# Kernel optimization log

Hardware: AMD Instinct MI355X
Metric: run time of the kernel (lower is better)

Reference implementation:

```python
import jax, jax.numpy as jnp
import numpy as np
from jax import lax

RATIOS = np.array([0.5, 1.0, 2.0], dtype=np.float32)
SCALES = np.array([8.0, 16.0, 32.0], dtype=np.float32)
BASE = 16.0
FEAT_STRIDE = 16
N_PRE_NMS = 6000
N_POST_NMS = 300
NMS_THRESH = 0.7
MIN_SIZE = 16.0
SCALE = 1.0
NEG_INF = -1e30


def generate_anchor_base():
    # (y1, x1, y2, x2) anchors centered at (BASE/2, BASE/2)
    h = BASE * SCALES[None, :] * np.sqrt(RATIOS)[:, None]          # [3,3]
    w = BASE * SCALES[None, :] * np.sqrt(1.0 / RATIOS)[:, None]
    cy = cx = BASE / 2.0
    ab = np.stack([cy - h / 2, cx - w / 2, cy + h / 2, cx + w / 2], axis=-1)
    return jnp.asarray(ab.reshape(-1, 4), dtype=jnp.float32)       # [9,4]


def enumerate_shift_anchor(anchor_base, hh, ww):
    sy = jnp.arange(hh, dtype=jnp.float32) * FEAT_STRIDE
    sx = jnp.arange(ww, dtype=jnp.float32) * FEAT_STRIDE
    mx, my = jnp.meshgrid(sx, sy)                                   # np.meshgrid(shift_x, shift_y)
    shift = jnp.stack([my.ravel(), mx.ravel(), my.ravel(), mx.ravel()], axis=1)  # [K,4]
    return (shift[:, None, :] + anchor_base[None, :, :]).reshape(-1, 4)          # [K*9,4]


def conv2d(x, w, b, pad):
    y = lax.conv_general_dilated(x, w, (1, 1), [(pad, pad), (pad, pad)],
                                 dimension_numbers=('NCHW', 'OIHW', 'NCHW'))
    return y + b[None, :, None, None]


def loc2bbox(anchor, loc):
    h = anchor[:, 2] - anchor[:, 0]
    w = anchor[:, 3] - anchor[:, 1]
    cy = anchor[:, 0] + 0.5 * h
    cx = anchor[:, 1] + 0.5 * w
    dy, dx, dh, dw = loc[:, 0], loc[:, 1], loc[:, 2], loc[:, 3]
    ncy = dy * h + cy
    ncx = dx * w + cx
    nh = jnp.exp(dh) * h
    nw = jnp.exp(dw) * w
    return jnp.stack([ncy - 0.5 * nh, ncx - 0.5 * nw, ncy + 0.5 * nh, ncx + 0.5 * nw], axis=1)


def nms_fixed(boxes, scores):
    # boxes [P,4] already score-sorted desc; greedy NMS, fixed N_POST_NMS outputs (zero-padded)
    def body(i, state):
        sc, keep = state
        idx = jnp.argmax(sc)
        valid = sc[idx] > NEG_INF / 2
        keep = keep.at[i].set(jnp.where(valid, idx, -1))
        box = boxes[idx]
        tl = jnp.maximum(box[:2], boxes[:, :2])
        br = jnp.minimum(box[2:], boxes[:, 2:])
        wh = jnp.clip(br - tl, 0.0)
        inter = wh[:, 0] * wh[:, 1]
        a1 = (box[2] - box[0]) * (box[3] - box[1])
        a2 = (boxes[:, 2] - boxes[:, 0]) * (boxes[:, 3] - boxes[:, 1])
        iou = inter / jnp.maximum(a1 + a2 - inter, 1e-6)
        sc = jnp.where(iou > NMS_THRESH, NEG_INF, sc)
        sc = sc.at[idx].set(NEG_INF)
        return sc, keep
    keep = jnp.full((N_POST_NMS,), -1, dtype=jnp.int32)
    _, keep = lax.fori_loop(0, N_POST_NMS, body, (scores, keep))
    rois = boxes[jnp.maximum(keep, 0)]
    return jnp.where(keep[:, None] >= 0, rois, 0.0)                # [N_POST,4]


def propose_one(loc, fg_score, anchor, img_h, img_w):
    roi = loc2bbox(anchor, loc)                                     # [A,4]
    roi = jnp.stack([jnp.clip(roi[:, 0], 0.0, img_h),
                     jnp.clip(roi[:, 1], 0.0, img_w),
                     jnp.clip(roi[:, 2], 0.0, img_h),
                     jnp.clip(roi[:, 3], 0.0, img_w)], axis=1)
    min_size = MIN_SIZE * SCALE
    hs = roi[:, 2] - roi[:, 0]
    ws = roi[:, 3] - roi[:, 1]
    valid = (hs >= min_size) & (ws >= min_size)
    sc = jnp.where(valid, fg_score, NEG_INF)
    top_sc, top_idx = lax.top_k(sc, N_PRE_NMS)
    return nms_fixed(roi[top_idx], top_sc)


def reference(x, conv1_w, conv1_b, score_w, score_b, loc_w, loc_b, img_h, img_w):
    n, _, hh, ww = x.shape
    anchor = enumerate_shift_anchor(generate_anchor_base(), hh, ww)  # [hh*ww*9,4]
    n_anchor = anchor.shape[0] // (hh * ww)
    feat = jax.nn.relu(conv2d(x, conv1_w, conv1_b, 1))
    rpn_locs = conv2d(feat, loc_w, loc_b, 0).transpose(0, 2, 3, 1).reshape(n, -1, 4)
    rpn_scores = conv2d(feat, score_w, score_b, 0).transpose(0, 2, 3, 1)
    soft = jax.nn.softmax(rpn_scores.reshape(n, hh, ww, n_anchor, 2), axis=4)
    rpn_fg = soft[..., 1].reshape(n, -1)
    rpn_scores = rpn_scores.reshape(n, -1, 2)
    rois = jax.vmap(lambda l, s: propose_one(l, s, anchor, float(img_h), float(img_w)))(rpn_locs, rpn_fg)
    return rpn_locs, rpn_scores, rois, anchor


def setup_inputs() -> dict:
    key = jax.random.key(0)
    ks = jax.random.split(key, 4)
    return {
        'x': jax.random.normal(ks[0], (4, 512, 64, 64), dtype=jnp.float32),
        'conv1_w': jax.random.normal(ks[1], (512, 512, 3, 3), dtype=jnp.float32) * 0.01,
        'conv1_b': jnp.zeros((512,), dtype=jnp.float32),
        'score_w': jax.random.normal(ks[2], (18, 512, 1, 1), dtype=jnp.float32) * 0.01,
        'score_b': jnp.zeros((18,), dtype=jnp.float32),
        'loc_w': jax.random.normal(ks[3], (36, 512, 1, 1), dtype=jnp.float32) * 0.01,
        'loc_b': jnp.zeros((36,), dtype=jnp.float32),
        'img_h': 1024,
        'img_w': 1024,
    }
```

## Files before the change

kernel.cpp:

```cpp
#include <hip/hip_runtime.h>
#include <stdint.h>

typedef unsigned int u32;
typedef unsigned long long u64;
typedef unsigned short ushort_t;

#define NANCH 36864
#define NPRE 6000
#define NPOST 300
#define CAP 6144
#define NKEEP 6000
#define MROWS 6016
#define MW 192
#define NEG_INF_F (-1e30f)

typedef __attribute__((ext_vector_type(8))) __bf16 bf8_t;
typedef __attribute__((ext_vector_type(8))) unsigned short us8_t;
typedef __attribute__((ext_vector_type(16))) float f32x16;

union pun8 { us8_t u; bf8_t b; };

__device__ __forceinline__ u32 fsort(float f) {
    u32 u = __float_as_uint(f);
    return (u & 0x80000000u) ? ~u : (u | 0x80000000u);
}

__device__ __forceinline__ unsigned short f2bf(float f) {
    u32 u = __float_as_uint(f);
    u32 r = (u + 0x7FFFu + ((u >> 16) & 1u)) >> 16;
    return (unsigned short)r;
}
__device__ __forceinline__ float bf2f(unsigned short s) {
    return __uint_as_float(((u32)s) << 16);
}

__device__ __forceinline__ int ctz32(u32 x) {
    return __builtin_ctz(x ? x : 1u);
}

__global__ void init_k(u32* cnt) {
    if (threadIdx.x < 8) cnt[threadIdx.x] = 0u;
}

__global__ void wpack_k(const float* __restrict__ w, ushort_t* __restrict__ Wp) {
    int T = blockIdx.x * 256 + threadIdx.x;
    if (T >= 32768) return;
    int lane31 = T & 31;
    int cot    = (T >> 5) & 15;
    int khalf  = (T >> 9) & 1;
    int kc     = T >> 10;
    int co  = cot * 32 + lane31;
    int ci0 = kc * 16 + khalf * 8;
    int lane = lane31 + khalf * 32;
    const float* wr = w + (size_t)co * 4608 + (size_t)ci0 * 9;
    us8_t* P = (us8_t*)Wp;
    const size_t sa_stride = (size_t)9 * 32 * 16 * 64;
#pragma unroll
    for (int t = 0; t < 9; ++t) {
        us8_t vh, vm, vl;
#pragma unroll
        for (int j = 0; j < 8; ++j) {
            float v = wr[j * 9 + t];
            unsigned short h = f2bf(v); float r1 = v - bf2f(h);
            unsigned short m = f2bf(r1); float r2 = r1 - bf2f(m);
            vh[j] = h; vm[j] = m; vl[j] = f2bf(r2);
        }
        size_t base = ((((size_t)t) * 32 + kc) * 16 + cot) * 64 + lane;
        P[base] = vh;
        P[base + sa_stride] = vm;
        P[base + 2 * sa_stride] = vl;
    }
}

__global__ void tw1_k(const float* __restrict__ sw, const float* __restrict__ lw,
                      float* __restrict__ wt1) {
    int i = blockIdx.x * 256 + threadIdx.x;
    if (i >= 512 * 64) return;
    int ci = i >> 6;
    int ch = i & 63;
    float v = 0.f;
    if (ch < 18) v = sw[ch * 512 + ci];
    else if (ch < 54) v = lw[(ch - 18) * 512 + ci];
    wt1[i] = v;
}

__global__ __launch_bounds__(256, 2) void conv_mfma_k(const float* __restrict__ x,
                                                      const ushort_t* __restrict__ Wp,
                                                      const float* __restrict__ bias,
                                                      float* __restrict__ feat,
                                                      int img_base) {
    __shared__ __align__(16) unsigned short xs[3 * 6336];

    const int bid = blockIdx.x;
    const int xcd = bid & 7;
    const int rest = bid >> 3;
    const int rest_max = gridDim.x >> 3;
    const int coq = xcd >> 1;
    const int g = (xcd & 1) * rest_max + rest;
    const int fimg = g >> 5;
    const int hp = g & 31;
    const int n = img_base + fimg;
    const int h0 = hp * 2;

    const int tid = threadIdx.x;
    const int lane = tid & 63;
    const int wv = tid >> 6;
    const int r = wv >> 1;
    const int wb = (wv & 1) * 32;
    const int col31 = lane & 31;
    const int halfk = lane >> 5;

    f32x16 acc[4];
#pragma unroll
    for (int q = 0; q < 4; ++q)
#pragma unroll
        for (int i = 0; i < 16; ++i) acc[q][i] = 0.f;

    const us8_t* Pw = (const us8_t*)Wp;
    const size_t sa_stride = (size_t)9 * 32 * 16 * 64;
    static const int sal[6] = {0, 0, 1, 0, 1, 2};
    static const int sbl[6] = {0, 1, 0, 2, 1, 0};

    for (int kc = 0; kc < 32; ++kc) {
        for (int e = tid; e < 528; e += 256) {
            int half = e & 1;
            int rc = e >> 1;
            int rr = rc / 66;
            int cc = rc - rr * 66;
            int gr = h0 + rr - 1;
            int gc = cc - 1;
            bool inb = ((unsigned)gr < 64u) && ((unsigned)gc < 64u);
            int ci0 = kc * 16 + half * 8;
            const float* xp = x + ((((size_t)n * 512 + ci0) * 64 + gr) * 64 + gc);
            us8_t vh, vm, vl;
#pragma unroll
            for (int j = 0; j < 8; ++j) {
                float v = inb ? xp[(size_t)j * 4096] : 0.f;
                unsigned short h = f2bf(v); float r1 = v - bf2f(h);
                unsigned short m = f2bf(r1); float r2 = r1 - bf2f(m);
                vh[j] = h; vm[j] = m; vl[j] = f2bf(r2);
            }
            int off = (rr * 66 + cc) * 24 + half * 8;
            *(us8_t*)&xs[off] = vh;
            *(us8_t*)&xs[6336 + off] = vm;
            *(us8_t*)&xs[12672 + off] = vl;
        }
        __syncthreads();

#pragma unroll
        for (int t = 0; t < 9; ++t) {
            const int kh = t / 3, kw = t - kh * 3;
            pun8 Bf[3];
            int boff = ((r + kh) * 66 + (wb + col31 + kw)) * 24 + halfk * 8;
#pragma unroll
            for (int sb = 0; sb < 3; ++sb)
                Bf[sb].u = *(const us8_t*)&xs[sb * 6336 + boff];
            pun8 Af[3][4];
            size_t abase = (((size_t)t * 32 + kc) * 16 + coq * 4) * 64 + lane;
#pragma unroll
            for (int sa = 0; sa < 3; ++sa)
#pragma unroll
                for (int q = 0; q < 4; ++q)
                    Af[sa][q].u = Pw[sa * sa_stride + abase + (size_t)q * 64];
#pragma unroll
            for (int pp = 0; pp < 6; ++pp) {
                const int sa = sal[pp], sb = sbl[pp];
#pragma unroll
                for (int q = 0; q < 4; ++q)
                    acc[q] = __builtin_amdgcn_mfma_f32_32x32x16_bf16(
                        Af[sa][q].b, Bf[sb].b, acc[q], 0, 0, 0);
            }
        }
        __syncthreads();
    }

#pragma unroll
    for (int q = 0; q < 4; ++q) {
#pragma unroll
        for (int i = 0; i < 16; ++i) {
            int m = (i & 3) + 8 * (i >> 2) + 4 * halfk;
            int co = coq * 128 + q * 32 + m;
            float v = acc[q][i] + bias[co];
            v = v > 0.f ? v : 0.f;
            feat[(((size_t)fimg * 512 + co) * 64 + (h0 + r)) * 64 + (wb + col31)] = v;
        }
    }
}

__global__ __launch_bounds__(64) void head_k(const float* __restrict__ feat,
                                             const float* __restrict__ wt1,
                                             const float* __restrict__ sb,
                                             const float* __restrict__ lb,
                                             const int* __restrict__ img_h,
                                             const int* __restrict__ img_w,
                                             float* __restrict__ out_loc,
                                             float* __restrict__ out_sc,
                                             float* __restrict__ boxes,
                                             float* __restrict__ scf,
                                             int img_base) {
    const int lane = threadIdx.x;
    const int row = blockIdx.x;
    const int fimg = blockIdx.y;
    const int n = img_base + fimg;

    float acc[56];
#pragma unroll
    for (int i = 0; i < 56; i++) acc[i] = 0.f;

    for (int ci = 0; ci < 512; ++ci) {
        float f = feat[(((size_t)fimg * 512 + ci) * 64 + row) * 64 + lane];
        const float4* wp = (const float4*)(wt1 + ci * 64);
#pragma unroll
        for (int q = 0; q < 14; q++) {
            float4 w4 = wp[q];
            acc[q * 4 + 0] = fmaf(f, w4.x, acc[q * 4 + 0]);
            acc[q * 4 + 1] = fmaf(f, w4.y, acc[q * 4 + 1]);
            acc[q * 4 + 2] = fmaf(f, w4.z, acc[q * 4 + 2]);
            acc[q * 4 + 3] = fmaf(f, w4.w, acc[q * 4 + 3]);
        }
    }

    float ihf = (float)img_h[0];
    float iwf = (float)img_w[0];
    int p = row * 64 + lane;
    size_t base = (size_t)n * NANCH + (size_t)p * 9;
    float sy = 16.f * (float)row;
    float sx = 16.f * (float)lane;
    const float rat[3] = {0.5f, 1.f, 2.f};
    const float scl[3] = {8.f, 16.f, 32.f};

#pragma unroll
    for (int a = 0; a < 9; a++) {
        int rr = a / 3, s = a % 3;
        float hh = 16.f * scl[s] * sqrtf(rat[rr]);
        float wwv = 16.f * scl[s] * sqrtf(1.f / rat[rr]);
        float ab0 = 8.f - 0.5f * hh, ab1 = 8.f - 0.5f * wwv;
        float ab2 = 8.f + 0.5f * hh, ab3 = 8.f + 0.5f * wwv;
        float a0 = sy + ab0, a1c = sx + ab1, a2 = sy + ab2, a3 = sx + ab3;

        float s0 = acc[a * 2 + 0] + sb[a * 2 + 0];
        float s1 = acc[a * 2 + 1] + sb[a * 2 + 1];
        ((float2*)out_sc)[base + a] = make_float2(s0, s1);
        float m = fmaxf(s0, s1);
        float e0 = expf(s0 - m), e1 = expf(s1 - m);
        float fg = e1 / (e0 + e1);

        float dy = acc[18 + a * 4 + 0] + lb[a * 4 + 0];
        float dx = acc[18 + a * 4 + 1] + lb[a * 4 + 1];
        float dh = acc[18 + a * 4 + 2] + lb[a * 4 + 2];
        float dw = acc[18 + a * 4 + 3] + lb[a * 4 + 3];
        ((float4*)out_loc)[base + a] = make_float4(dy, dx, dh, dw);

        float h_ = a2 - a0, w_ = a3 - a1c;
        float cy = a0 + 0.5f * h_, cx = a1c + 0.5f * w_;
        float ncy = dy * h_ + cy, ncx = dx * w_ + cx;
        float nh = expf(dh) * h_, nw = expf(dw) * w_;
        float y1 = ncy - 0.5f * nh, x1 = ncx - 0.5f * nw;
        float y2 = ncy + 0.5f * nh, x2 = ncx + 0.5f * nw;
        y1 = fminf(fmaxf(y1, 0.f), ihf);
        x1 = fminf(fmaxf(x1, 0.f), iwf);
        y2 = fminf(fmaxf(y2, 0.f), ihf);
        x2 = fminf(fmaxf(x2, 0.f), iwf);
        float hs = y2 - y1, wsz = x2 - x1;
        bool valid = (hs >= 16.f) && (wsz >= 16.f);
        ((float4*)boxes)[base + a] = make_float4(y1, x1, y2, x2);
        scf[base + a] = valid ? fg : NEG_INF_F;
    }
}

__global__ void anch_k(float* __restrict__ out_anchor) {
    int i = blockIdx.x * 256 + threadIdx.x;
    if (i >= NANCH) return;
    int p = i / 9, a = i - p * 9;
    int y = p / 64, xq = p - y * 64;
    int r = a / 3, s = a - r * 3;
    const float rat[3] = {0.5f, 1.f, 2.f};
    const float scl[3] = {8.f, 16.f, 32.f};
    float hh = 16.f * scl[s] * sqrtf(rat[r]);
    float wwv = 16.f * scl[s] * sqrtf(1.f / rat[r]);
    float ab0 = 8.f - 0.5f * hh, ab1 = 8.f - 0.5f * wwv;
    float ab2 = 8.f + 0.5f * hh, ab3 = 8.f + 0.5f * wwv;
    float sy = 16.f * (float)y, sx = 16.f * (float)xq;
    ((float4*)out_anchor)[i] = make_float4(sy + ab0, sx + ab1, sy + ab2, sx + ab3);
}

__global__ __launch_bounds__(1024) void radix_k(const float* __restrict__ scf, u32* __restrict__ uT) {
    const int b = blockIdx.x;
    const int tid = threadIdx.x;
    const float* s = scf + (size_t)b * NANCH;
    __shared__ u32 hist[256];
    __shared__ u32 sel_prefix;
    __shared__ int sel_rank;
    if (tid == 0) { sel_prefix = 0u; sel_rank = NPRE; }
    __syncthreads();
    for (int p = 3; p >= 0; --p) {
        for (int i = tid; i < 256; i += 1024) hist[i] = 0u;
        __syncthreads();
        u32 prefix = sel_prefix;
        u32 highmask = (p == 3) ? 0u : (0xFFFFFFFFu << ((p + 1) * 8));
        for (int i = tid; i < NANCH; i += 1024) {
            u32 u = fsort(s[i]);
            if ((u & highmask) == prefix)
                atomicAdd(&hist[(u >> (p * 8)) & 255], 1u);
        }
        __syncthreads();
        if (tid == 0) {
            int r = sel_rank;
            u32 accum = 0;
            int bsel = 0;
            for (int bb = 255; bb >= 0; --bb) {
                accum += hist[bb];
                if ((int)accum >= r) {
                    bsel = bb;
                    sel_rank = r - (int)(accum - hist[bb]);
                    break;
                }
            }
            sel_prefix = prefix | ((u32)bsel << (p * 8));
        }
        __syncthreads();
    }
    if (tid == 0) uT[b] = sel_prefix;
}

__global__ void compact_k(const float* __restrict__ scf, const u32* __restrict__ uT,
                          u32* __restrict__ cnt, u32* __restrict__ cidx) {
    int b = blockIdx.y;
    int i = blockIdx.x * 256 + threadIdx.x;
    float s = scf[(size_t)b * NANCH + i];
    u32 u = fsort(s);
    if (u >= uT[b] && s > -5e29f) {
        u32 p = atomicAdd(&cnt[b], 1u);
        if (p < CAP) cidx[(size_t)b * CAP + p] = (u32)i;
    }
}

__global__ __launch_bounds__(1024) void sort_k(const float* __restrict__ scf,
                                               const float* __restrict__ boxes,
                                               u32* __restrict__ cnt,
                                               const u32* __restrict__ cidx,
                                               float4* __restrict__ sbox) {
    __shared__ u64 sk[8192];
    const int b = blockIdx.x;
    const int tid = threadIdx.x;
    int count = (int)cnt[b];
    if (count > CAP) count = CAP;

    for (int i = tid; i < 8192; i += 1024) {
        u64 key = 0ull;
        if (i < count) {
            u32 idx = cidx[(size_t)b * CAP + i];
            u32 u = fsort(scf[(size_t)b * NANCH + idx]);
            key = ((u64)u << 32) | (u64)(0xFFFFFFFFu - idx);
        }
        sk[i] = key;
    }

    for (int k = 2; k <= 8192; k <<= 1) {
        for (int j = k >> 1; j > 0; j >>= 1) {
            __syncthreads();
            for (int i = tid; i < 8192; i += 1024) {
                int p = i ^ j;
                if (p > i) {
                    bool up = (i & k) == 0;
                    u64 a = sk[i], c = sk[p];
                    bool sw = up ? (a < c) : (a > c);
                    if (sw) { sk[i] = c; sk[p] = a; }
                }
            }
        }
    }
    __syncthreads();

    int S = count < NKEEP ? count : NKEEP;
    if (tid == 0) cnt[4 + b] = (u32)S;
    const float4* Bx = (const float4*)boxes;
    for (int i = tid; i < S; i += 1024) {
        u32 idx = 0xFFFFFFFFu - (u32)(sk[i] & 0xFFFFFFFFull);
        sbox[(size_t)b * CAP + i] = Bx[(size_t)b * NANCH + idx];
    }
}

__global__ __launch_bounds__(256) void mask_k(const float4* __restrict__ sbox,
                                              const u32* __restrict__ cnt,
                                              u32* __restrict__ mask) {
    __shared__ float4 rb[64];
    __shared__ float ra[64];
    const int tile = blockIdx.x;
    const int b = blockIdx.y;
    const int tid = threadIdx.x;
    const int lane = tid & 63;
    const int wv = tid >> 6;
    const int r0 = tile * 64;

    if (tid < 64) {
        float4 v = sbox[(size_t)b * CAP + (r0 + tid)];
        rb[tid] = v;
        ra[tid] = (v.z - v.x) * (v.w - v.y);
    }
    __syncthreads();

    for (int chunk = (tile >> 2); chunk < 24; ++chunk) {
        int c = chunk * 256 + tid;
        float4 cb = sbox[(size_t)b * CAP + c];
        float a2 = (cb.z - cb.x) * (cb.w - cb.y);
        u64 mine = 0ull;
#pragma unroll 4
        for (int r = 0; r < 64; ++r) {
            float4 rr = rb[r];
            float ty = fmaxf(rr.x, cb.x);
            float tx = fmaxf(rr.y, cb.y);
            float by = fminf(rr.z, cb.z);
            float bx = fminf(rr.w, cb.w);
            float ih = fmaxf(by - ty, 0.f);
            float iw = fmaxf(bx - tx, 0.f);
            float inter = ih * iw;
            float iou = inter / fmaxf(ra[r] + a2 - inter, 1e-6f);
            u64 bal = __ballot(iou > 0.7f);
            if (lane == r) mine = bal;
        }
        int row = r0 + lane;
        u64* dst = (u64*)(mask + ((size_t)b * MROWS + row) * MW);
        dst[chunk * 4 + wv] = mine;
    }
}

__global__ __launch_bounds__(64) void scan_k(const u32* __restrict__ mask,
                                             const float4* __restrict__ sbox,
                                             const u32* __restrict__ cnt,
                                             float4* __restrict__ out_rois) {
    const int b = blockIdx.x;
    const int lane = threadIdx.x;
    const int S = (int)cnt[4 + b];

    __shared__ int keep[NPOST];

    u32 a0, a1, a2v;
    {
        int w;
        w = lane;       a0  = (w * 32 + 32 <= S) ? 0xFFFFFFFFu : ((w * 32 < S) ? ((1u << (S - w * 32)) - 1u) : 0u);
        w = 64 + lane;  a1  = (w * 32 + 32 <= S) ? 0xFFFFFFFFu : ((w * 32 < S) ? ((1u << (S - w * 32)) - 1u) : 0u);
        w = 128 + lane; a2v = (w * 32 + 32 <= S) ? 0xFFFFFFFFu : ((w * 32 < S) ? ((1u << (S - w * 32)) - 1u) : 0u);
    }

    const u32* mbase = mask + (size_t)b * MROWS * MW;
    int it = 0;
    while (it < NPOST) {
        int j;
        u64 b0 = __ballot(a0 != 0u);
        if (b0) {
            int L = __builtin_ctzll(b0);
            int cv = (lane << 5) + ctz32(a0);
            j = __shfl(cv, L);
        } else {
            u64 b1 = __ballot(a1 != 0u);
            if (b1) {
                int L = __builtin_ctzll(b1);
                int cv = ((64 + lane) << 5) + ctz32(a1);
                j = __shfl(cv, L);
            } else {
                u64 b2 = __ballot(a2v != 0u);
                if (!b2) break;
                int L = __builtin_ctzll(b2);
                int cv = ((128 + lane) << 5) + ctz32(a2v);
                j = __shfl(cv, L);
            }
        }
        if (lane == 0) keep[it] = j;
        ++it;

        int wj = j >> 5;
        u32 bit = 1u << (j & 31);
        if (wj == lane) a0 &= ~bit;
        else if (wj == 64 + lane) a1 &= ~bit;
        else if (wj == 128 + lane) a2v &= ~bit;

        const u32* row = mbase + (size_t)j * MW;
        u32 m0 = row[lane];
        u32 m1 = row[64 + lane];
        u32 m2 = row[128 + lane];
        a0 &= ~m0; a1 &= ~m1; a2v &= ~m2;
    }

    __syncthreads();

    int total = it;
    for (int i = lane; i < NPOST; i += 64) {
        float4 v = make_float4(0.f, 0.f, 0.f, 0.f);
        if (i < total) v = sbox[(size_t)b * CAP + keep[i]];
        out_rois[(size_t)b * NPOST + i] = v;
    }
}

extern "C" void kernel_launch(void* const* d_in, const int* in_sizes, int n_in,
                              void* d_out, int out_size, void* d_ws, size_t ws_size,
                              hipStream_t stream) {
    const float* x  = (const float*)d_in[0];
    const float* w1 = (const float*)d_in[1];
    const float* b1 = (const float*)d_in[2];
    const float* sw = (const float*)d_in[3];
    const float* sb = (const float*)d_in[4];
    const float* lw = (const float*)d_in[5];
    const float* lb = (const float*)d_in[6];
    const int* ih   = (const int*)d_in[7];
    const int* iw   = (const int*)d_in[8];
    float* out = (float*)d_out;

    char* ws = (char*)d_ws;
    const size_t FEAT_OFF = 14286848;
    const size_t NEED_BIG = 51413504;
    const bool big = (ws_size >= NEED_BIG);

    ushort_t* Wp  = (ushort_t*)(ws);
    float* feat   = (float*)(ws + FEAT_OFF);
    u32* mask     = (u32*)(ws);
    const size_t RB = big ? (FEAT_OFF + 33554432) : (FEAT_OFF + 16777216);
    float* wt1    = (float*)(ws + RB);
    float* boxes  = (float*)(ws + RB + 131072);
    float* scf    = (float*)(ws + RB + 2490368);
    u32* uT       = (u32*)(ws + RB + 3080192);
    u32* cnt      = (u32*)(ws + RB + 3080448);
    u32* cidx     = (u32*)(ws + RB + 3080704);
    float4* sbox  = (float4*)(ws + RB + 3179008);

    float* out_loc = out;
    float* out_sc  = out + 589824;
    float4* out_roi = (float4*)(out + 884736);
    float* out_anc = out + 889536;

    hipLaunchKernelGGL(init_k, dim3(1), dim3(64), 0, stream, cnt);
    hipLaunchKernelGGL(wpack_k, dim3(128), dim3(256), 0, stream, w1, Wp);
    hipLaunchKernelGGL(tw1_k, dim3(128), dim3(256), 0, stream, sw, lw, wt1);
    hipLaunchKernelGGL(anch_k, dim3(144), dim3(256), 0, stream, out_anc);

    if (big) {
        hipLaunchKernelGGL(conv_mfma_k, dim3(512), dim3(256), 0, stream, x, Wp, b1, feat, 0);
        hipLaunchKernelGGL(head_k, dim3(64, 4), dim3(64), 0, stream, feat, wt1, sb, lb, ih, iw,
                           out_loc, out_sc, boxes, scf, 0);
    } else {
        for (int pass = 0; pass < 2; ++pass) {
            hipLaunchKernelGGL(conv_mfma_k, dim3(256), dim3(256), 0, stream, x, Wp, b1, feat, pass * 2);
            hipLaunchKernelGGL(head_k, dim3(64, 2), dim3(64), 0, stream, feat, wt1, sb, lb, ih, iw,
                               out_loc, out_sc, boxes, scf, pass * 2);
        }
    }

    hipLaunchKernelGGL(radix_k, dim3(4), dim3(1024), 0, stream, scf, uT);
    hipLaunchKernelGGL(compact_k, dim3(144, 4), dim3(256), 0, stream, scf, uT, cnt, cidx);
    hipLaunchKernelGGL(sort_k, dim3(4), dim3(1024), 0, stream, scf, boxes, cnt, cidx, sbox);
    hipLaunchKernelGGL(mask_k, dim3(94, 4), dim3(256), 0, stream, sbox, cnt, mask);
    hipLaunchKernelGGL(scan_k, dim3(4), dim3(64), 0, stream, mask, sbox, cnt, out_roi);
}
```

Before: 1.171 ms.

## Fuse setup kernels, retile conv warps to 2x2, add mask-prefetch warps to NMS scan

Merges the four small setup kernels (weight pack, head weight transpose, anchors, counter init) into one launch to cut launch overhead. Changes the conv warp tiling so each warp covers 64 output channels by two 32-pixel column halves instead of 128 channels by one half. This halves the A-fragment global loads per warp at the cost of two B-fragment LDS reads. Adds 15 helper warps to the serial NMS scan that read mask rows ahead of the leader's current position, warming the cache for its dependent row loads. They spin with s_sleep on a volatile shared position and write a dummy sink so the loads are not removed.

```diff
diff --git a/kernel.cpp b/kernel.cpp
--- a/kernel.cpp
+++ b/kernel.cpp
@@ -38,50 +38,65 @@
     return __builtin_ctz(x ? x : 1u);
 }
 
-__global__ void init_k(u32* cnt) {
-    if (threadIdx.x < 8) cnt[threadIdx.x] = 0u;
-}
-
-__global__ void wpack_k(const float* __restrict__ w, ushort_t* __restrict__ Wp) {
-    int T = blockIdx.x * 256 + threadIdx.x;
-    if (T >= 32768) return;
-    int lane31 = T & 31;
-    int cot    = (T >> 5) & 15;
-    int khalf  = (T >> 9) & 1;
-    int kc     = T >> 10;
-    int co  = cot * 32 + lane31;
-    int ci0 = kc * 16 + khalf * 8;
-    int lane = lane31 + khalf * 32;
-    const float* wr = w + (size_t)co * 4608 + (size_t)ci0 * 9;
-    us8_t* P = (us8_t*)Wp;
-    const size_t sa_stride = (size_t)9 * 32 * 16 * 64;
-#pragma unroll
-    for (int t = 0; t < 9; ++t) {
-        us8_t vh, vm, vl;
-#pragma unroll
-        for (int j = 0; j < 8; ++j) {
-            float v = wr[j * 9 + t];
-            unsigned short h = f2bf(v); float r1 = v - bf2f(h);
-            unsigned short m = f2bf(r1); float r2 = r1 - bf2f(m);
-            vh[j] = h; vm[j] = m; vl[j] = f2bf(r2);
-        }
-        size_t base = ((((size_t)t) * 32 + kc) * 16 + cot) * 64 + lane;
-        P[base] = vh;
-        P[base + sa_stride] = vm;
-        P[base + 2 * sa_stride] = vl;
-    }
-}
-
-__global__ void tw1_k(const float* __restrict__ sw, const float* __restrict__ lw,
-                      float* __restrict__ wt1) {
-    int i = blockIdx.x * 256 + threadIdx.x;
-    if (i >= 512 * 64) return;
-    int ci = i >> 6;
-    int ch = i & 63;
-    float v = 0.f;
-    if (ch < 18) v = sw[ch * 512 + ci];
-    else if (ch < 54) v = lw[(ch - 18) * 512 + ci];
-    wt1[i] = v;
+__global__ void setup_k(const float* __restrict__ w1, const float* __restrict__ sw,
+                        const float* __restrict__ lw, ushort_t* __restrict__ Wp,
+                        float* __restrict__ wt1, float* __restrict__ out_anchor,
+                        u32* __restrict__ cnt) {
+    const int bid = blockIdx.x;
+    const int tid = threadIdx.x;
+    if (bid < 128) {
+        int T = bid * 256 + tid;
+        int lane31 = T & 31;
+        int cot    = (T >> 5) & 15;
+        int khalf  = (T >> 9) & 1;
+        int kc     = T >> 10;
+        int co  = cot * 32 + lane31;
+        int ci0 = kc * 16 + khalf * 8;
+        int lane = lane31 + khalf * 32;
+        const float* wr = w1 + (size_t)co * 4608 + (size_t)ci0 * 9;
+        us8_t* P = (us8_t*)Wp;
+        const size_t sa_stride = (size_t)9 * 32 * 16 * 64;
+#pragma unroll
+        for (int t = 0; t < 9; ++t) {
+            us8_t vh, vm, vl;
+#pragma unroll
+            for (int j = 0; j < 8; ++j) {
+                float v = wr[j * 9 + t];
+                unsigned short h = f2bf(v); float r1 = v - bf2f(h);
+                unsigned short m = f2bf(r1); float r2 = r1 - bf2f(m);
+                vh[j] = h; vm[j] = m; vl[j] = f2bf(r2);
+            }
+            size_t base = ((((size_t)t) * 32 + kc) * 16 + cot) * 64 + lane;
+            P[base] = vh;
+            P[base + sa_stride] = vm;
+            P[base + 2 * sa_stride] = vl;
+        }
+    } else if (bid < 256) {
+        int i = (bid - 128) * 256 + tid;
+        int ci = i >> 6;
+        int ch = i & 63;
+        float v = 0.f;
+        if (ch < 18) v = sw[ch * 512 + ci];
+        else if (ch < 54) v = lw[(ch - 18) * 512 + ci];
+        wt1[i] = v;
+    } else if (bid < 400) {
+        int i = (bid - 256) * 256 + tid;
+        if (i < NANCH) {
+            int p = i / 9, a = i - p * 9;
+            int y = p / 64, xq = p - y * 64;
+            int r = a / 3, s = a - r * 3;
+            const float rat[3] = {0.5f, 1.f, 2.f};
+            const float scl[3] = {8.f, 16.f, 32.f};
+            float hh = 16.f * scl[s] * sqrtf(rat[r]);
+            float wwv = 16.f * scl[s] * sqrtf(1.f / rat[r]);
+            float ab0 = 8.f - 0.5f * hh, ab1 = 8.f - 0.5f * wwv;
+            float ab2 = 8.f + 0.5f * hh, ab3 = 8.f + 0.5f * wwv;
+            float sy = 16.f * (float)y, sx = 16.f * (float)xq;
+            ((float4*)out_anchor)[i] = make_float4(sy + ab0, sx + ab1, sy + ab2, sx + ab3);
+        }
+    } else {
+        if (tid < 8) cnt[tid] = 0u;
+    }
 }
 
 __global__ __launch_bounds__(256, 2) void conv_mfma_k(const float* __restrict__ x,
@@ -105,8 +120,8 @@
     const int tid = threadIdx.x;
     const int lane = tid & 63;
     const int wv = tid >> 6;
-    const int r = wv >> 1;
-    const int wb = (wv & 1) * 32;
+    const int r = wv & 1;
+    const int coh = (wv >> 1);
     const int col31 = lane & 31;
     const int halfk = lane >> 5;
 
@@ -150,41 +165,46 @@
 #pragma unroll
         for (int t = 0; t < 9; ++t) {
             const int kh = t / 3, kw = t - kh * 3;
-            pun8 Bf[3];
-            int boff = ((r + kh) * 66 + (wb + col31 + kw)) * 24 + halfk * 8;
+            pun8 Bf[3][2];
+            int boff0 = ((r + kh) * 66 + (col31 + kw)) * 24 + halfk * 8;
 #pragma unroll
             for (int sb = 0; sb < 3; ++sb)
-                Bf[sb].u = *(const us8_t*)&xs[sb * 6336 + boff];
-            pun8 Af[3][4];
-            size_t abase = (((size_t)t * 32 + kc) * 16 + coq * 4) * 64 + lane;
+#pragma unroll
+                for (int ps = 0; ps < 2; ++ps)
+                    Bf[sb][ps].u = *(const us8_t*)&xs[sb * 6336 + boff0 + ps * (32 * 24)];
+            pun8 Af[3][2];
+            size_t abase = (((size_t)t * 32 + kc) * 16 + coq * 4 + coh * 2) * 64 + lane;
 #pragma unroll
             for (int sa = 0; sa < 3; ++sa)
 #pragma unroll
-                for (int q = 0; q < 4; ++q)
-                    Af[sa][q].u = Pw[sa * sa_stride + abase + (size_t)q * 64];
+                for (int cs = 0; cs < 2; ++cs)
+                    Af[sa][cs].u = Pw[sa * sa_stride + abase + (size_t)cs * 64];
 #pragma unroll
             for (int pp = 0; pp < 6; ++pp) {
                 const int sa = sal[pp], sb = sbl[pp];
 #pragma unroll
-                for (int q = 0; q < 4; ++q)
-                    acc[q] = __builtin_amdgcn_mfma_f32_32x32x16_bf16(
-                        Af[sa][q].b, Bf[sb].b, acc[q], 0, 0, 0);
+                for (int cs = 0; cs < 2; ++cs)
+#pragma unroll
+                    for (int ps = 0; ps < 2; ++ps)
+                        acc[cs * 2 + ps] = __builtin_amdgcn_mfma_f32_32x32x16_bf16(
+                            Af[sa][cs].b, Bf[sb][ps].b, acc[cs * 2 + ps], 0, 0, 0);
             }
         }
         __syncthreads();
     }
 
 #pragma unroll
-    for (int q = 0; q < 4; ++q) {
-#pragma unroll
-        for (int i = 0; i < 16; ++i) {
-            int m = (i & 3) + 8 * (i >> 2) + 4 * halfk;
-            int co = coq * 128 + q * 32 + m;
-            float v = acc[q][i] + bias[co];
-            v = v > 0.f ? v : 0.f;
-            feat[(((size_t)fimg * 512 + co) * 64 + (h0 + r)) * 64 + (wb + col31)] = v;
-        }
-    }
+    for (int cs = 0; cs < 2; ++cs)
+#pragma unroll
+        for (int ps = 0; ps < 2; ++ps)
+#pragma unroll
+            for (int i = 0; i < 16; ++i) {
+                int m = (i & 3) + 8 * (i >> 2) + 4 * halfk;
+                int co = coq * 128 + coh * 64 + cs * 32 + m;
+                float v = acc[cs * 2 + ps][i] + bias[co];
+                v = v > 0.f ? v : 0.f;
+                feat[(((size_t)fimg * 512 + co) * 64 + (h0 + r)) * 64 + (ps * 32 + col31)] = v;
+            }
 }
 
 __global__ __launch_bounds__(64) void head_k(const float* __restrict__ feat,
@@ -266,22 +286,6 @@
         ((float4*)boxes)[base + a] = make_float4(y1, x1, y2, x2);
         scf[base + a] = valid ? fg : NEG_INF_F;
     }
-}
-
-__global__ void anch_k(float* __restrict__ out_anchor) {
-    int i = blockIdx.x * 256 + threadIdx.x;
-    if (i >= NANCH) return;
-    int p = i / 9, a = i - p * 9;
-    int y = p / 64, xq = p - y * 64;
-    int r = a / 3, s = a - r * 3;
-    const float rat[3] = {0.5f, 1.f, 2.f};
-    const float scl[3] = {8.f, 16.f, 32.f};
-    float hh = 16.f * scl[s] * sqrtf(rat[r]);
-    float wwv = 16.f * scl[s] * sqrtf(1.f / rat[r]);
-    float ab0 = 8.f - 0.5f * hh, ab1 = 8.f - 0.5f * wwv;
-    float ab2 = 8.f + 0.5f * hh, ab3 = 8.f + 0.5f * wwv;
-    float sy = 16.f * (float)y, sx = 16.f * (float)xq;
-    ((float4*)out_anchor)[i] = make_float4(sy + ab0, sx + ab1, sy + ab2, sx + ab3);
 }
 
 __global__ __launch_bounds__(1024) void radix_k(const float* __restrict__ scf, u32* __restrict__ uT) {
@@ -425,70 +429,91 @@
     }
 }
 
-__global__ __launch_bounds__(64) void scan_k(const u32* __restrict__ mask,
-                                             const float4* __restrict__ sbox,
-                                             const u32* __restrict__ cnt,
-                                             float4* __restrict__ out_rois) {
+__global__ __launch_bounds__(1024) void scan_k(const u32* __restrict__ mask,
+                                               const float4* __restrict__ sbox,
+                                               const u32* __restrict__ cnt,
+                                               u32* __restrict__ sink,
+                                               float4* __restrict__ out_rois) {
     const int b = blockIdx.x;
-    const int lane = threadIdx.x;
+    const int tid = threadIdx.x;
+    const int wv = tid >> 6;
+    const int lane = tid & 63;
     const int S = (int)cnt[4 + b];
 
     __shared__ int keep[NPOST];
-
-    u32 a0, a1, a2v;
-    {
-        int w;
-        w = lane;       a0  = (w * 32 + 32 <= S) ? 0xFFFFFFFFu : ((w * 32 < S) ? ((1u << (S - w * 32)) - 1u) : 0u);
-        w = 64 + lane;  a1  = (w * 32 + 32 <= S) ? 0xFFFFFFFFu : ((w * 32 < S) ? ((1u << (S - w * 32)) - 1u) : 0u);
-        w = 128 + lane; a2v = (w * 32 + 32 <= S) ? 0xFFFFFFFFu : ((w * 32 < S) ? ((1u << (S - w * 32)) - 1u) : 0u);
-    }
+    __shared__ int posS;
+    volatile int* vpos = &posS;
+    if (tid == 0) *vpos = 0;
+    __syncthreads();
 
     const u32* mbase = mask + (size_t)b * MROWS * MW;
-    int it = 0;
-    while (it < NPOST) {
-        int j;
-        u64 b0 = __ballot(a0 != 0u);
-        if (b0) {
-            int L = __builtin_ctzll(b0);
-            int cv = (lane << 5) + ctz32(a0);
-            j = __shfl(cv, L);
-        } else {
-            u64 b1 = __ballot(a1 != 0u);
-            if (b1) {
-                int L = __builtin_ctzll(b1);
-                int cv = ((64 + lane) << 5) + ctz32(a1);
+
+    if (wv == 0) {
+        u32 a0, a1, a2v;
+        {
+            int w;
+            w = lane;       a0  = (w * 32 + 32 <= S) ? 0xFFFFFFFFu : ((w * 32 < S) ? ((1u << (S - w * 32)) - 1u) : 0u);
+            w = 64 + lane;  a1  = (w * 32 + 32 <= S) ? 0xFFFFFFFFu : ((w * 32 < S) ? ((1u << (S - w * 32)) - 1u) : 0u);
+            w = 128 + lane; a2v = (w * 32 + 32 <= S) ? 0xFFFFFFFFu : ((w * 32 < S) ? ((1u << (S - w * 32)) - 1u) : 0u);
+        }
+
+        int it = 0;
+        while (it < NPOST) {
+            int j;
+            u64 b0 = __ballot(a0 != 0u);
+            if (b0) {
+                int L = __builtin_ctzll(b0);
+                int cv = (lane << 5) + ctz32(a0);
                 j = __shfl(cv, L);
             } else {
-                u64 b2 = __ballot(a2v != 0u);
-                if (!b2) break;
-                int L = __builtin_ctzll(b2);
-                int cv = ((128 + lane) << 5) + ctz32(a2v);
-                j = __shfl(cv, L);
-            }
-        }
-        if (lane == 0) keep[it] = j;
-        ++it;
-
-        int wj = j >> 5;
-        u32 bit = 1u << (j & 31);
-        if (wj == lane) a0 &= ~bit;
-        else if (wj == 64 + lane) a1 &= ~bit;
-        else if (wj == 128 + lane) a2v &= ~bit;
-
-        const u32* row = mbase + (size_t)j * MW;
-        u32 m0 = row[lane];
-        u32 m1 = row[64 + lane];
-        u32 m2 = row[128 + lane];
-        a0 &= ~m0; a1 &= ~m1; a2v &= ~m2;
-    }
-
-    __syncthreads();
-
-    int total = it;
-    for (int i = lane; i < NPOST; i += 64) {
-        float4 v = make_float4(0.f, 0.f, 0.f, 0.f);
-        if (i < total) v = sbox[(size_t)b * CAP + keep[i]];
-        out_rois[(size_t)b * NPOST + i] = v;
+                u64 b1 = __ballot(a1 != 0u);
+                if (b1) {
+                    int L = __builtin_ctzll(b1);
+                    int cv = ((64 + lane) << 5) + ctz32(a1);
+                    j = __shfl(cv, L);
+                } else {
+                    u64 b2 = __ballot(a2v != 0u);
+                    if (!b2) break;
+                    int L = __builtin_ctzll(b2);
+                    int cv = ((128 + lane) << 5) + ctz32(a2v);
+                    j = __shfl(cv, L);
+                }
+            }
+            if (lane == 0) { keep[it] = j; *vpos = j; }
+            ++it;
+
+            int wj = j >> 5;
+            u32 bit = 1u << (j & 31);
+            if (wj == lane) a0 &= ~bit;
+            else if (wj == 64 + lane) a1 &= ~bit;
+            else if (wj == 128 + lane) a2v &= ~bit;
+
+            const u32* row = mbase + (size_t)j * MW;
+            u32 m0 = row[lane];
+            u32 m1 = row[64 + lane];
+            u32 m2 = row[128 + lane];
+            a0 &= ~m0; a1 &= ~m1; a2v &= ~m2;
+        }
+
+        if (lane == 0) *vpos = (1 << 28);
+
+        int total = it;
+        for (int i = lane; i < NPOST; i += 64) {
+            float4 v = make_float4(0.f, 0.f, 0.f, 0.f);
+            if (i < total) v = sbox[(size_t)b * CAP + keep[i]];
+            out_rois[(size_t)b * NPOST + i] = v;
+        }
+    } else {
+        u32 dummy = 0u;
+        const int W = 2048;
+        for (int r = wv - 1; r < MROWS; r += 15) {
+            int sp = 0;
+            while (*vpos + W <= r && sp < 65536) { __builtin_amdgcn_s_sleep(2); ++sp; }
+            if (*vpos >= (1 << 27)) break;
+            const u32* row = mbase + (size_t)r * MW;
+            dummy += row[lane] + row[64 + lane] + row[128 + lane];
+        }
+        if (dummy == 0xDEADBEEFu) sink[b] = dummy;
     }
 }
 
@@ -528,10 +553,7 @@
     float4* out_roi = (float4*)(out + 884736);
     float* out_anc = out + 889536;
 
-    hipLaunchKernelGGL(init_k, dim3(1), dim3(64), 0, stream, cnt);
-    hipLaunchKernelGGL(wpack_k, dim3(128), dim3(256), 0, stream, w1, Wp);
-    hipLaunchKernelGGL(tw1_k, dim3(128), dim3(256), 0, stream, sw, lw, wt1);
-    hipLaunchKernelGGL(anch_k, dim3(144), dim3(256), 0, stream, out_anc);
+    hipLaunchKernelGGL(setup_k, dim3(401), dim3(256), 0, stream, w1, sw, lw, Wp, wt1, out_anc, cnt);
 
     if (big) {
         hipLaunchKernelGGL(conv_mfma_k, dim3(512), dim3(256), 0, stream, x, Wp, b1, feat, 0);
@@ -549,5 +571,5 @@
     hipLaunchKernelGGL(compact_k, dim3(144, 4), dim3(256), 0, stream, scf, uT, cnt, cidx);
     hipLaunchKernelGGL(sort_k, dim3(4), dim3(1024), 0, stream, scf, boxes, cnt, cidx, sbox);
     hipLaunchKernelGGL(mask_k, dim3(94, 4), dim3(256), 0, stream, sbox, cnt, mask);
-    hipLaunchKernelGGL(scan_k, dim3(4), dim3(64), 0, stream, mask, sbox, cnt, out_roi);
-}
+    hipLaunchKernelGGL(scan_k, dim3(4), dim3(1024), 0, stream, mask, sbox, cnt, cidx, out_roi);
+}
```

Result: faster. 1.114 ms (-4.9%).
